# Kernel tuning notes

Measured on AMD Instinct MI355X. Metric: run time of the kernel, lower is better.

Reference implementation:

```python
import jax, jax.numpy as jnp
import numpy as np

MAX_SEQ = 2048
NUM_HEADS = 32
NUM_KV_HEADS = 4
HEAD_DIM = 256
HIDDEN = 4096
ROTARY_DIM = 64  # head_dim * partial_rotary_factor(0.25)
THETA = 10000000.0
EPS = 1e-6
GROUPS = NUM_HEADS // NUM_KV_HEADS
SCALE = 1.0 / np.sqrt(HEAD_DIM)


def rms_norm(x, w):
    xf = x.astype(jnp.float32)
    norm = jax.lax.rsqrt(jnp.mean(xf * xf, axis=-1, keepdims=True) + EPS)
    return (xf * norm * w).astype(x.dtype)


def partial_rope(x, position):
    # x: [B, H, 1, D]; rotate first ROTARY_DIM dims (split-half convention)
    half = ROTARY_DIM // 2
    inv_freq = 1.0 / (THETA ** (jnp.arange(half, dtype=jnp.float32) / half))
    freqs = position.astype(jnp.float32) * inv_freq  # [half]
    cos = jnp.cos(freqs).reshape(1, 1, 1, -1)
    sin = jnp.sin(freqs).reshape(1, 1, 1, -1)
    x1 = x[..., :half]
    x2 = x[..., half:ROTARY_DIM]
    x_pass = x[..., ROTARY_DIM:]
    rot = jnp.concatenate([x1 * cos - x2 * sin, x2 * cos + x1 * sin], axis=-1)
    return jnp.concatenate([rot, x_pass], axis=-1)


def setup_inputs() -> dict:
    key = jax.random.key(0)
    ks = jax.random.split(key, 10)
    pos = 1500
    position = jnp.array([pos], dtype=jnp.int32)
    idx = jnp.arange(MAX_SEQ)
    mask = jnp.where(idx <= pos, 0.0, -1e9).astype(jnp.float32).reshape(1, 1, 1, MAX_SEQ)
    onehot = (idx == pos).astype(jnp.float32).reshape(1, 1, MAX_SEQ, 1)
    return {
        "x": jax.random.normal(ks[0], (1, 1, HIDDEN), dtype=jnp.float32),
        "position": position,
        "mask": mask,
        "k_cache": jax.random.normal(ks[1], (1, NUM_KV_HEADS, MAX_SEQ, HEAD_DIM), dtype=jnp.float32),
        "v_cache": jax.random.normal(ks[2], (1, NUM_KV_HEADS, MAX_SEQ, HEAD_DIM), dtype=jnp.float32),
        "onehot": onehot,
        "q_proj_w": jax.random.normal(ks[3], (2 * NUM_HEADS * HEAD_DIM, HIDDEN), dtype=jnp.float32) * 0.02,
        "k_proj_w": jax.random.normal(ks[4], (NUM_KV_HEADS * HEAD_DIM, HIDDEN), dtype=jnp.float32) * 0.02,
        "v_proj_w": jax.random.normal(ks[5], (NUM_KV_HEADS * HEAD_DIM, HIDDEN), dtype=jnp.float32) * 0.02,
        "o_proj_w": jax.random.normal(ks[6], (HIDDEN, NUM_HEADS * HEAD_DIM), dtype=jnp.float32) * 0.02,
        "q_norm_w": jnp.ones((HEAD_DIM,), dtype=jnp.float32),
        "k_norm_w": jnp.ones((HEAD_DIM,), dtype=jnp.float32),
    }


def reference(x, position, mask, k_cache, v_cache, onehot,
              q_proj_w, k_proj_w, v_proj_w, o_proj_w, q_norm_w, k_norm_w):
    B, T, _ = x.shape  # B=T=1
    # Q + gate interleaved per head
    qg = jnp.einsum('bth,oh->bto', x, q_proj_w).reshape(B, T, NUM_HEADS, 2 * HEAD_DIM)
    q = qg[..., :HEAD_DIM]                      # [B,T,H,D]
    gate = qg[..., HEAD_DIM:].reshape(B, T, -1)  # [B,T,H*D]
    q = jnp.transpose(q, (0, 2, 1, 3))           # [B,H,T,D]
    k = jnp.einsum('bth,oh->bto', x, k_proj_w).reshape(B, T, NUM_KV_HEADS, HEAD_DIM).transpose(0, 2, 1, 3)
    v = jnp.einsum('bth,oh->bto', x, v_proj_w).reshape(B, T, NUM_KV_HEADS, HEAD_DIM).transpose(0, 2, 1, 3)
    q = rms_norm(q, q_norm_w)
    k = rms_norm(k, k_norm_w)
    q = partial_rope(q, position)
    k = partial_rope(k, position)
    # full-buffer onehot cache update (same math as mul_/add_)
    k_cache = k_cache * (1.0 - onehot) + k * onehot  # [B,KV,S,D]
    v_cache = v_cache * (1.0 - onehot) + v * onehot
    # GQA: group query heads over kv heads without materializing expanded KV
    qg_heads = q.reshape(B, NUM_KV_HEADS, GROUPS, T, HEAD_DIM)
    attn = jnp.einsum('bgktd,bgsd->bgkts', qg_heads, k_cache) * SCALE  # [B,KV,G,T,S]
    attn = attn + mask[:, :, None]  # mask [B,1,1,T,S] broadcast
    attn = jax.nn.softmax(attn, axis=-1)
    out = jnp.einsum('bgkts,bgsd->bgktd', attn, v_cache)  # [B,KV,G,T,D]
    out = out.reshape(B, NUM_HEADS, T, HEAD_DIM).transpose(0, 2, 1, 3).reshape(B, T, -1)
    out = out * jax.nn.sigmoid(gate)
    return jnp.einsum('bto,ho->bth', out, o_proj_w)
```

## Files before the change

### kernel.cpp

```cpp
#include <hip/hip_runtime.h>
#include <math.h>

#define MAX_SEQ   2048
#define NUM_HEADS 32
#define NUM_KV    4
#define HEAD_DIM  256
#define HIDDEN    4096
#define ROT_DIM   64
#define GROUPS    8
#define SCALE     0.0625f
#define CHUNK     32
#define NCHUNK    (MAX_SEQ / CHUNK)

typedef float f4 __attribute__((ext_vector_type(4)));

__device__ inline f4 ntload4(const float* p) {
    return __builtin_nontemporal_load(reinterpret_cast<const f4*>(p));
}

__global__ __launch_bounds__(256) void gemv_qkv(
    const float* __restrict__ x,
    const float* __restrict__ qw,
    const float* __restrict__ kw,
    const float* __restrict__ vw,
    float* __restrict__ out)
{
    const int wave = threadIdx.x >> 6;
    const int lane = threadIdx.x & 63;
    const int row  = blockIdx.x * 4 + wave;

    const float* w;
    if (row < 16384)      w = qw + (size_t)row * HIDDEN;
    else if (row < 17408) w = kw + (size_t)(row - 16384) * HIDDEN;
    else                  w = vw + (size_t)(row - 17408) * HIDDEN;

    float acc = 0.f;
#pragma unroll
    for (int it = 0; it < HIDDEN / 256; ++it) {
        const int idx = it * 256 + lane * 4;
        f4 wv = ntload4(w + idx);
        f4 xv = *reinterpret_cast<const f4*>(x + idx);
        acc += wv[0] * xv[0] + wv[1] * xv[1] + wv[2] * xv[2] + wv[3] * xv[3];
    }
#pragma unroll
    for (int off = 32; off >= 1; off >>= 1) acc += __shfl_xor(acc, off);
    if (lane == 0) out[row] = acc;
}

__global__ __launch_bounds__(256) void norm_rope(
    const float* __restrict__ qkv,
    const float* __restrict__ qnw,
    const float* __restrict__ knw,
    const int*   __restrict__ posp,
    float* __restrict__ qf,
    float* __restrict__ kf)
{
    const int h = blockIdx.x;
    const int d = threadIdx.x;
    const bool is_q = (h < NUM_HEADS);
    const float* src = is_q ? (qkv + h * 512)
                            : (qkv + 16384 + (h - NUM_HEADS) * HEAD_DIM);
    const float val = src[d];

    __shared__ float red[4];
    float ss = val * val;
#pragma unroll
    for (int off = 32; off >= 1; off >>= 1) ss += __shfl_xor(ss, off);
    if ((threadIdx.x & 63) == 0) red[threadIdx.x >> 6] = ss;
    __syncthreads();
    const float tot  = red[0] + red[1] + red[2] + red[3];
    const float norm = rsqrtf(tot * (1.0f / HEAD_DIM) + 1e-6f);
    const float wgt  = is_q ? qnw[d] : knw[d];
    const float nv   = val * norm * wgt;

    __shared__ float buf[HEAD_DIM];
    buf[d] = nv;
    __syncthreads();

    float outv = nv;
    if (d < ROT_DIM) {
        const int i = d & 31;
        const int pos = posp[0];
        const double inv_freq = pow(10000000.0, -(double)i / 32.0);
        const double ang = (double)pos * inv_freq;
        const float c = (float)cos(ang);
        const float s = (float)sin(ang);
        const float x1 = buf[i];
        const float x2 = buf[i + 32];
        outv = (d < 32) ? (x1 * c - x2 * s) : (x2 * c + x1 * s);
    }
    float* dst = is_q ? (qf + h * HEAD_DIM) : (kf + (h - NUM_HEADS) * HEAD_DIM);
    dst[d] = outv;
}

__global__ __launch_bounds__(256) void attn_partial(
    const float* __restrict__ qf,
    const float* __restrict__ kcache,
    const float* __restrict__ vcache,
    const float* __restrict__ kf,
    const float* __restrict__ vnew,
    const int*   __restrict__ posp,
    float* __restrict__ part_m,
    float* __restrict__ part_l,
    float* __restrict__ part_acc)
{
    const int kv  = blockIdx.x;
    const int c   = blockIdx.y;
    const int pos = posp[0];
    const int s0  = c * CHUNK;
    const int s1  = min(s0 + CHUNK, pos + 1);
    const int tid = threadIdx.x;

    if (s0 > pos) {
        if (tid == 0) {
#pragma unroll
            for (int g = 0; g < GROUPS; ++g) {
                const int pid = (kv * GROUPS + g) * NCHUNK + c;
                part_m[pid] = -1e30f; part_l[pid] = 0.f;
            }
        }
        return;
    }

    const float* kbase = kcache + (size_t)kv * MAX_SEQ * HEAD_DIM;
    const float* vbase = vcache + (size_t)kv * MAX_SEQ * HEAD_DIM;

    const int lane = tid & 63;
    const int wave = tid >> 6;

    f4 q8[GROUPS];
#pragma unroll
    for (int g = 0; g < GROUPS; ++g)
        q8[g] = *reinterpret_cast<const f4*>(qf + (kv * GROUPS + g) * HEAD_DIM + lane * 4);

    __shared__ float sc[GROUPS][CHUNK];
    __shared__ float pl[GROUPS][CHUNK];
    __shared__ float mh[GROUPS], lh[GROUPS];

    for (int i = wave; i < CHUNK; i += 4) {
        const int s = s0 + i;
        float part[GROUPS];
#pragma unroll
        for (int g = 0; g < GROUPS; ++g) part[g] = 0.f;
        const bool valid = (s < s1);
        if (valid) {
            const float* krow = (s == pos) ? (kf + kv * HEAD_DIM)
                                           : (kbase + (size_t)s * HEAD_DIM);
            f4 kvec = *reinterpret_cast<const f4*>(krow + lane * 4);
#pragma unroll
            for (int g = 0; g < GROUPS; ++g) {
                f4 t = q8[g] * kvec;
                part[g] += t[0] + t[1] + t[2] + t[3];
            }
        }
#pragma unroll
        for (int off = 32; off >= 1; off >>= 1) {
#pragma unroll
            for (int g = 0; g < GROUPS; ++g)
                part[g] += __shfl_xor(part[g], off);
        }
        if (lane == 0) {
#pragma unroll
            for (int g = 0; g < GROUPS; ++g)
                sc[g][i] = valid ? part[g] * SCALE : -1e30f;
        }
    }
    __syncthreads();

    {
        const int h = tid >> 5;
        const int j = tid & 31;
        float v = sc[h][j];
        float m = v;
#pragma unroll
        for (int off = 16; off >= 1; off >>= 1)
            m = fmaxf(m, __shfl_xor(m, off));
        const float p = expf(v - m);
        pl[h][j] = p;
        float ls = p;
#pragma unroll
        for (int off = 16; off >= 1; off >>= 1)
            ls += __shfl_xor(ls, off);
        if (j == 0) { mh[h] = m; lh[h] = ls; }
    }
    __syncthreads();

    const int d = tid;
    float acc[GROUPS];
#pragma unroll
    for (int g = 0; g < GROUPS; ++g) acc[g] = 0.f;
    for (int s = s0; s < s1; ++s) {
        const float* vrow = (s == pos) ? (vnew + kv * HEAD_DIM)
                                       : (vbase + (size_t)s * HEAD_DIM);
        const float v = vrow[d];
        const int i = s - s0;
#pragma unroll
        for (int g = 0; g < GROUPS; ++g) acc[g] += pl[g][i] * v;
    }
#pragma unroll
    for (int g = 0; g < GROUPS; ++g) {
        const int pid = (kv * GROUPS + g) * NCHUNK + c;
        part_acc[(size_t)pid * HEAD_DIM + d] = acc[g];
        if (tid == 0) { part_m[pid] = mh[g]; part_l[pid] = lh[g]; }
    }
}

__global__ __launch_bounds__(256) void attn_combine(
    const float* __restrict__ part_m,
    const float* __restrict__ part_l,
    const float* __restrict__ part_acc,
    const float* __restrict__ qkv,
    float* __restrict__ attn_gated)
{
    const int h = blockIdx.x;
    const int d = threadIdx.x;

    float M = -1e30f;
    for (int c = 0; c < NCHUNK; ++c) M = fmaxf(M, part_m[h * NCHUNK + c]);

    float L = 0.f, acc = 0.f;
    for (int c = 0; c < NCHUNK; ++c) {
        const float lc = part_l[h * NCHUNK + c];
        if (lc > 0.f) {
            const float w = expf(part_m[h * NCHUNK + c] - M);
            L   += lc * w;
            acc += part_acc[(size_t)(h * NCHUNK + c) * HEAD_DIM + d] * w;
        }
    }
    const float o   = acc / L;
    const float g   = qkv[h * 512 + 256 + d];
    const float sig = 1.0f / (1.0f + expf(-g));
    attn_gated[h * HEAD_DIM + d] = o * sig;
}

__global__ __launch_bounds__(256) void gemv_o(
    const float* __restrict__ vec,
    const float* __restrict__ w,
    float* __restrict__ out)
{
    const int wave = threadIdx.x >> 6;
    const int lane = threadIdx.x & 63;
    const int row  = blockIdx.x * 4 + wave;
    const float* wr = w + (size_t)row * 8192;

    float acc = 0.f;
#pragma unroll
    for (int it = 0; it < 8192 / 256; ++it) {
        const int idx = it * 256 + lane * 4;
        f4 wv = ntload4(wr + idx);
        f4 xv = *reinterpret_cast<const f4*>(vec + idx);
        acc += wv[0] * xv[0] + wv[1] * xv[1] + wv[2] * xv[2] + wv[3] * xv[3];
    }
#pragma unroll
    for (int off = 32; off >= 1; off >>= 1) acc += __shfl_xor(acc, off);
    if (lane == 0) out[row] = acc;
}

extern "C" void kernel_launch(void* const* d_in, const int* in_sizes, int n_in,
                              void* d_out, int out_size, void* d_ws, size_t ws_size,
                              hipStream_t stream) {
    const float* x        = (const float*)d_in[0];
    const int*   position = (const int*)  d_in[1];
    const float* k_cache  = (const float*)d_in[3];
    const float* v_cache  = (const float*)d_in[4];
    const float* q_proj_w = (const float*)d_in[6];
    const float* k_proj_w = (const float*)d_in[7];
    const float* v_proj_w = (const float*)d_in[8];
    const float* o_proj_w = (const float*)d_in[9];
    const float* q_norm_w = (const float*)d_in[10];
    const float* k_norm_w = (const float*)d_in[11];
    float* out = (float*)d_out;

    float* ws         = (float*)d_ws;
    float* qkv        = ws;
    float* qf         = ws + 18432;
    float* kf         = ws + 26624;
    float* part_m     = ws + 27648;
    float* part_l     = ws + 29696;
    float* part_acc   = ws + 31744;
    float* attn_gated = ws + 556032;

    gemv_qkv<<<18432 / 4, 256, 0, stream>>>(x, q_proj_w, k_proj_w, v_proj_w, qkv);
    norm_rope<<<NUM_HEADS + NUM_KV, 256, 0, stream>>>(qkv, q_norm_w, k_norm_w,
                                                      position, qf, kf);
    dim3 g3(NUM_KV, NCHUNK);
    attn_partial<<<g3, 256, 0, stream>>>(qf, k_cache, v_cache, kf, qkv + 17408,
                                         position, part_m, part_l, part_acc);
    attn_combine<<<NUM_HEADS, 256, 0, stream>>>(part_m, part_l, part_acc, qkv,
                                                attn_gated);
    gemv_o<<<4096 / 4, 256, 0, stream>>>(attn_gated, o_proj_w, out);
}
```

Measured before the change: 108.8 us.

## Fuse norm/rope into attention and use one block per GEMV row

Removes the separate norm_rope kernel: each attention block now recomputes RMS norm and partial RoPE for its 8 query heads plus the KV head from the qkv buffer, keeping results in shared memory. Both GEMV kernels switch from one wave per row to a full 256-thread block per row, with a shared-memory reduction at the end. K/V cache reads now use nontemporal loads. This saves a launch and a global round trip, but the per-row block layout adds many more blocks and a __syncthreads per row. The norm and RoPE work is also duplicated across all 64 chunk blocks.

```diff
diff --git a/kernel.cpp b/kernel.cpp
--- a/kernel.cpp
+++ b/kernel.cpp
@@ -25,9 +25,8 @@
     const float* __restrict__ vw,
     float* __restrict__ out)
 {
-    const int wave = threadIdx.x >> 6;
-    const int lane = threadIdx.x & 63;
-    const int row  = blockIdx.x * 4 + wave;
+    const int row = blockIdx.x;
+    const int tid = threadIdx.x;
 
     const float* w;
     if (row < 16384)      w = qw + (size_t)row * HIDDEN;
@@ -36,69 +35,26 @@
 
     float acc = 0.f;
 #pragma unroll
-    for (int it = 0; it < HIDDEN / 256; ++it) {
-        const int idx = it * 256 + lane * 4;
-        f4 wv = ntload4(w + idx);
-        f4 xv = *reinterpret_cast<const f4*>(x + idx);
+    for (int j = 0; j < 4; ++j) {
+        const int col = j * 1024 + tid * 4;
+        f4 wv = ntload4(w + col);
+        f4 xv = *reinterpret_cast<const f4*>(x + col);
         acc += wv[0] * xv[0] + wv[1] * xv[1] + wv[2] * xv[2] + wv[3] * xv[3];
     }
 #pragma unroll
     for (int off = 32; off >= 1; off >>= 1) acc += __shfl_xor(acc, off);
-    if (lane == 0) out[row] = acc;
-}
-
-__global__ __launch_bounds__(256) void norm_rope(
+    __shared__ float red[4];
+    if ((tid & 63) == 0) red[tid >> 6] = acc;
+    __syncthreads();
+    if (tid == 0) out[row] = red[0] + red[1] + red[2] + red[3];
+}
+
+__global__ __launch_bounds__(256) void attn_partial(
     const float* __restrict__ qkv,
     const float* __restrict__ qnw,
     const float* __restrict__ knw,
-    const int*   __restrict__ posp,
-    float* __restrict__ qf,
-    float* __restrict__ kf)
-{
-    const int h = blockIdx.x;
-    const int d = threadIdx.x;
-    const bool is_q = (h < NUM_HEADS);
-    const float* src = is_q ? (qkv + h * 512)
-                            : (qkv + 16384 + (h - NUM_HEADS) * HEAD_DIM);
-    const float val = src[d];
-
-    __shared__ float red[4];
-    float ss = val * val;
-#pragma unroll
-    for (int off = 32; off >= 1; off >>= 1) ss += __shfl_xor(ss, off);
-    if ((threadIdx.x & 63) == 0) red[threadIdx.x >> 6] = ss;
-    __syncthreads();
-    const float tot  = red[0] + red[1] + red[2] + red[3];
-    const float norm = rsqrtf(tot * (1.0f / HEAD_DIM) + 1e-6f);
-    const float wgt  = is_q ? qnw[d] : knw[d];
-    const float nv   = val * norm * wgt;
-
-    __shared__ float buf[HEAD_DIM];
-    buf[d] = nv;
-    __syncthreads();
-
-    float outv = nv;
-    if (d < ROT_DIM) {
-        const int i = d & 31;
-        const int pos = posp[0];
-        const double inv_freq = pow(10000000.0, -(double)i / 32.0);
-        const double ang = (double)pos * inv_freq;
-        const float c = (float)cos(ang);
-        const float s = (float)sin(ang);
-        const float x1 = buf[i];
-        const float x2 = buf[i + 32];
-        outv = (d < 32) ? (x1 * c - x2 * s) : (x2 * c + x1 * s);
-    }
-    float* dst = is_q ? (qf + h * HEAD_DIM) : (kf + (h - NUM_HEADS) * HEAD_DIM);
-    dst[d] = outv;
-}
-
-__global__ __launch_bounds__(256) void attn_partial(
-    const float* __restrict__ qf,
     const float* __restrict__ kcache,
     const float* __restrict__ vcache,
-    const float* __restrict__ kf,
-    const float* __restrict__ vnew,
     const int*   __restrict__ posp,
     float* __restrict__ part_m,
     float* __restrict__ part_l,
@@ -108,7 +64,6 @@
     const int c   = blockIdx.y;
     const int pos = posp[0];
     const int s0  = c * CHUNK;
-    const int s1  = min(s0 + CHUNK, pos + 1);
     const int tid = threadIdx.x;
 
     if (s0 > pos) {
@@ -121,17 +76,76 @@
         }
         return;
     }
+    const int s1 = min(s0 + CHUNK, pos + 1);
+
+    const int lane = tid & 63;
+    const int wave = tid >> 6;
+    const int d    = tid;
+
+    float vals[9];
+#pragma unroll
+    for (int g = 0; g < GROUPS; ++g)
+        vals[g] = qkv[(kv * GROUPS + g) * 512 + d];
+    vals[8] = qkv[16384 + kv * HEAD_DIM + d];
+
+    __shared__ float ssred[9][4];
+    {
+        float sq[9];
+#pragma unroll
+        for (int g = 0; g < 9; ++g) sq[g] = vals[g] * vals[g];
+#pragma unroll
+        for (int off = 32; off >= 1; off >>= 1) {
+#pragma unroll
+            for (int g = 0; g < 9; ++g) sq[g] += __shfl_xor(sq[g], off);
+        }
+        if (lane == 0) {
+#pragma unroll
+            for (int g = 0; g < 9; ++g) ssred[g][wave] = sq[g];
+        }
+    }
+    __syncthreads();
+
+    __shared__ __align__(16) float qn[9][HEAD_DIM];
+    {
+        const float qw_ = qnw[d];
+        const float kw_ = knw[d];
+#pragma unroll
+        for (int g = 0; g < 9; ++g) {
+            const float tot  = ssred[g][0] + ssred[g][1] + ssred[g][2] + ssred[g][3];
+            const float norm = rsqrtf(tot * (1.0f / HEAD_DIM) + 1e-6f);
+            qn[g][d] = vals[g] * norm * (g < 8 ? qw_ : kw_);
+        }
+    }
+    __syncthreads();
+
+    if (d < ROT_DIM) {
+        const int i = d & 31;
+        const double inv_freq = pow(10000000.0, -(double)i / 32.0);
+        const double ang = (double)pos * inv_freq;
+        const float co = (float)cos(ang);
+        const float si = (float)sin(ang);
+        float rv[9];
+#pragma unroll
+        for (int g = 0; g < 9; ++g) {
+            const float x1 = qn[g][i];
+            const float x2 = qn[g][i + 32];
+            rv[g] = (d < 32) ? (x1 * co - x2 * si) : (x2 * co + x1 * si);
+        }
+        __syncthreads();
+#pragma unroll
+        for (int g = 0; g < 9; ++g) qn[g][d] = rv[g];
+    } else {
+        __syncthreads();
+    }
+    __syncthreads();
 
     const float* kbase = kcache + (size_t)kv * MAX_SEQ * HEAD_DIM;
     const float* vbase = vcache + (size_t)kv * MAX_SEQ * HEAD_DIM;
 
-    const int lane = tid & 63;
-    const int wave = tid >> 6;
-
     f4 q8[GROUPS];
 #pragma unroll
     for (int g = 0; g < GROUPS; ++g)
-        q8[g] = *reinterpret_cast<const f4*>(qf + (kv * GROUPS + g) * HEAD_DIM + lane * 4);
+        q8[g] = *reinterpret_cast<const f4*>(&qn[g][lane * 4]);
 
     __shared__ float sc[GROUPS][CHUNK];
     __shared__ float pl[GROUPS][CHUNK];
@@ -144,9 +158,9 @@
         for (int g = 0; g < GROUPS; ++g) part[g] = 0.f;
         const bool valid = (s < s1);
         if (valid) {
-            const float* krow = (s == pos) ? (kf + kv * HEAD_DIM)
-                                           : (kbase + (size_t)s * HEAD_DIM);
-            f4 kvec = *reinterpret_cast<const f4*>(krow + lane * 4);
+            f4 kvec;
+            if (s == pos) kvec = *reinterpret_cast<const f4*>(&qn[8][lane * 4]);
+            else          kvec = ntload4(kbase + (size_t)s * HEAD_DIM + lane * 4);
 #pragma unroll
             for (int g = 0; g < GROUPS; ++g) {
                 f4 t = q8[g] * kvec;
@@ -185,14 +199,13 @@
     }
     __syncthreads();
 
-    const int d = tid;
     float acc[GROUPS];
 #pragma unroll
     for (int g = 0; g < GROUPS; ++g) acc[g] = 0.f;
+    const float* vnew = qkv + 17408 + kv * HEAD_DIM;
     for (int s = s0; s < s1; ++s) {
-        const float* vrow = (s == pos) ? (vnew + kv * HEAD_DIM)
-                                       : (vbase + (size_t)s * HEAD_DIM);
-        const float v = vrow[d];
+        const float v = (s == pos) ? vnew[d]
+                                   : __builtin_nontemporal_load(vbase + (size_t)s * HEAD_DIM + d);
         const int i = s - s0;
 #pragma unroll
         for (int g = 0; g < GROUPS; ++g) acc[g] += pl[g][i] * v;
@@ -238,22 +251,24 @@
     const float* __restrict__ w,
     float* __restrict__ out)
 {
-    const int wave = threadIdx.x >> 6;
-    const int lane = threadIdx.x & 63;
-    const int row  = blockIdx.x * 4 + wave;
+    const int row = blockIdx.x;
+    const int tid = threadIdx.x;
     const float* wr = w + (size_t)row * 8192;
 
     float acc = 0.f;
 #pragma unroll
-    for (int it = 0; it < 8192 / 256; ++it) {
-        const int idx = it * 256 + lane * 4;
-        f4 wv = ntload4(wr + idx);
-        f4 xv = *reinterpret_cast<const f4*>(vec + idx);
+    for (int j = 0; j < 8; ++j) {
+        const int col = j * 1024 + tid * 4;
+        f4 wv = ntload4(wr + col);
+        f4 xv = *reinterpret_cast<const f4*>(vec + col);
         acc += wv[0] * xv[0] + wv[1] * xv[1] + wv[2] * xv[2] + wv[3] * xv[3];
     }
 #pragma unroll
     for (int off = 32; off >= 1; off >>= 1) acc += __shfl_xor(acc, off);
-    if (lane == 0) out[row] = acc;
+    __shared__ float red[4];
+    if ((tid & 63) == 0) red[tid >> 6] = acc;
+    __syncthreads();
+    if (tid == 0) out[row] = red[0] + red[1] + red[2] + red[3];
 }
 
 extern "C" void kernel_launch(void* const* d_in, const int* in_sizes, int n_in,
@@ -273,20 +288,17 @@
 
     float* ws         = (float*)d_ws;
     float* qkv        = ws;
-    float* qf         = ws + 18432;
-    float* kf         = ws + 26624;
-    float* part_m     = ws + 27648;
-    float* part_l     = ws + 29696;
-    float* part_acc   = ws + 31744;
-    float* attn_gated = ws + 556032;
-
-    gemv_qkv<<<18432 / 4, 256, 0, stream>>>(x, q_proj_w, k_proj_w, v_proj_w, qkv);
-    norm_rope<<<NUM_HEADS + NUM_KV, 256, 0, stream>>>(qkv, q_norm_w, k_norm_w,
-                                                      position, qf, kf);
-    dim3 g3(NUM_KV, NCHUNK);
-    attn_partial<<<g3, 256, 0, stream>>>(qf, k_cache, v_cache, kf, qkv + 17408,
-                                         position, part_m, part_l, part_acc);
+    float* part_m     = ws + 18432;
+    float* part_l     = ws + 20480;
+    float* part_acc   = ws + 22528;
+    float* attn_gated = ws + 546816;
+
+    gemv_qkv<<<18432, 256, 0, stream>>>(x, q_proj_w, k_proj_w, v_proj_w, qkv);
+    dim3 g2(NUM_KV, NCHUNK);
+    attn_partial<<<g2, 256, 0, stream>>>(qkv, q_norm_w, k_norm_w,
+                                         k_cache, v_cache, position,
+                                         part_m, part_l, part_acc);
     attn_combine<<<NUM_HEADS, 256, 0, stream>>>(part_m, part_l, part_acc, qkv,
                                                 attn_gated);
-    gemv_o<<<4096 / 4, 256, 0, stream>>>(attn_gated, o_proj_w, out);
-}
+    gemv_o<<<4096, 256, 0, stream>>>(attn_gated, o_proj_w, out);
+}
```

New measurement: 113.0 us. 3.8% more time.
